# Kernel tuning notes

Hardware: AMD Instinct MI355X
Metric: run time of the kernel (lower is better)

The kernel has to match this reference:

```python
import jax, jax.numpy as jnp
import numpy as np


def bilinear_resize(x, out_h, out_w):
    # x: [B, C, H, W]; matches torch F.interpolate(mode='bilinear', align_corners=False)
    B, C, H, W = x.shape
    ry = jnp.clip((jnp.arange(out_h, dtype=jnp.float32) + 0.5) * (H / out_h) - 0.5, 0.0, H - 1)
    rx = jnp.clip((jnp.arange(out_w, dtype=jnp.float32) + 0.5) * (W / out_w) - 0.5, 0.0, W - 1)
    y0 = jnp.floor(ry).astype(jnp.int32); y1 = jnp.minimum(y0 + 1, H - 1)
    x0 = jnp.floor(rx).astype(jnp.int32); x1 = jnp.minimum(x0 + 1, W - 1)
    wy = (ry - y0)[:, None]  # [out_h,1]
    wx = (rx - x0)[None, :]  # [1,out_w]
    r0 = x[:, :, y0, :]; r1 = x[:, :, y1, :]
    v00 = r0[:, :, :, x0]; v01 = r0[:, :, :, x1]
    v10 = r1[:, :, :, x0]; v11 = r1[:, :, :, x1]
    return (v00 * (1 - wx) + v01 * wx) * (1 - wy) + (v10 * (1 - wx) + v11 * wx) * wy


def setup_inputs() -> dict:
    key0 = jax.random.key(0)
    ks = jax.random.split(key0, 16)
    B, N, C, H = 2, 300, 256, 8
    hw_lvl = np.array([[64, 64], [32, 32], [16, 16]], dtype=np.int64)
    L = int((hw_lvl[:, 0] * hw_lvl[:, 1]).sum())  # 5376
    p = lambda k, sh: (0.02 * jax.random.normal(k, sh, dtype=jnp.float32))
    return {
        'query': jax.random.normal(ks[0], (B, N, C), dtype=jnp.float32),
        'key': jax.random.normal(ks[1], (B, L, C), dtype=jnp.float32),
        'value': jax.random.normal(ks[2], (B, L, C), dtype=jnp.float32),
        'key_padding_mask': jnp.zeros((B, L), dtype=bool),
        'hw_lvl': hw_lvl,
        'Wq': p(ks[3], (C, C)), 'Wk': p(ks[4], (C, C)), 'Wv': p(ks[5], (C, C)),
        'Wp': p(ks[6], (C, C)), 'bp': jnp.zeros((C,), jnp.float32),
        'W1': p(ks[7], (H, H)), 'b1': jnp.zeros((H,), jnp.float32),
        'W2': p(ks[8], (H, H)), 'b2': jnp.zeros((H,), jnp.float32),
        'W3': p(ks[9], (H, H)), 'b3': jnp.zeros((H,), jnp.float32),
        'Wm': p(ks[10], (3 * H, 1)), 'bm': jnp.zeros((1,), jnp.float32),
    }


def reference(query, key, value, key_padding_mask, hw_lvl,
              Wq, Wk, Wv, Wp, bp, W1, b1, W2, b2, W3, b3, Wm, bm):
    hw = np.asarray(hw_lvl)
    h1, wd1 = int(hw[0, 0]), int(hw[0, 1])
    h2, wd2 = int(hw[1, 0]), int(hw[1, 1])
    h3, wd3 = int(hw[2, 0]), int(hw[2, 1])
    w1 = h1 * wd1
    w2 = w1 + h2 * wd2
    B, N, C = query.shape
    L = key.shape[1]
    H = W1.shape[0]
    scale = (C // H) ** -0.5

    q = (query @ Wq).reshape(B, N, H, C // H)
    k = (key @ Wk).reshape(B, L, H, C // H)
    v = (value @ Wv).reshape(B, L, H, C // H)
    attn = jnp.einsum('bnhd,blhd->bhnl', q, k) * scale  # [B,H,N,L]

    ap = attn.transpose(0, 2, 3, 1)  # [B,N,L,H]
    f1 = jax.nn.relu(ap[:, :, :w1] @ W1 + b1)                      # [B,N,w1,H]
    f2 = jax.nn.relu(ap[:, :, w1:w2] @ W2 + b2)                    # [B,N,h2*wd2,H]
    f3 = jax.nn.relu(ap[:, :, w2:] @ W3 + b3)                      # [B,N,h3*wd3,H]
    f2 = f2.transpose(0, 1, 3, 2).reshape(B * N, H, h2, wd2)
    f3 = f3.transpose(0, 1, 3, 2).reshape(B * N, H, h3, wd3)
    f2 = bilinear_resize(f2, h1, wd1).transpose(0, 2, 3, 1).reshape(B, N, w1, H)
    f3 = bilinear_resize(f3, h1, wd1).transpose(0, 2, 3, 1).reshape(B, N, w1, H)
    new_feats = jnp.concatenate([f1, f2, f3], axis=-1)             # [B,N,w1,3H]
    mask = jax.nn.relu(new_feats @ Wm + bm)                        # [B,N,w1,1]

    aw = jax.nn.softmax(attn, axis=-1)                             # [B,H,N,L]
    x = jnp.einsum('bhnl,blhd->bnhd', aw, v).reshape(B, N, C)
    x = x @ Wp + bp
    return x, mask
```

## Files before the change

kernel.cpp:

```cpp
#include <hip/hip_runtime.h>
#include <hip/hip_bf16.h>

typedef __hip_bfloat16 bf16;
typedef __attribute__((ext_vector_type(8))) short short8v;
typedef __attribute__((ext_vector_type(8))) unsigned short ushort8v;
typedef __attribute__((ext_vector_type(4))) unsigned short ushort4v;
typedef __attribute__((ext_vector_type(4))) float float4v;

__device__ __forceinline__ float bfu2f(unsigned short u) {
    union { unsigned int i; float f; } v; v.i = ((unsigned int)u) << 16; return v.f;
}
__device__ __forceinline__ unsigned short f2bfu_rn(float x) {
    union { float f; unsigned int i; } u; u.f = x;
    unsigned int r = (u.i + 0x7FFFu + ((u.i >> 16) & 1u)) >> 16;
    return (unsigned short)r;
}

__global__ __launch_bounds__(256) void cast_wt(
    const float* __restrict__ Wq, const float* __restrict__ Wk,
    const float* __restrict__ Wv, const float* __restrict__ Wp,
    unsigned short* __restrict__ wt)
{
    __shared__ unsigned short tile[64][72];
    const float* W = (blockIdx.z == 0) ? Wq : (blockIdx.z == 1) ? Wk
                   : (blockIdx.z == 2) ? Wv : Wp;
    unsigned short* WT = wt + (size_t)blockIdx.z * 65536;
    const int t = threadIdx.x;
    const int k0 = blockIdx.x * 64, n0 = blockIdx.y * 64;
    {
        const int r = t >> 2, cseg = (t & 3) * 16;
        const float* src = W + (size_t)(k0 + r) * 256 + n0 + cseg;
        #pragma unroll
        for (int j = 0; j < 16; ++j) tile[r][cseg + j] = f2bfu_rn(src[j]);
    }
    __syncthreads();
    {
        const int ch = t & 63, lq = t >> 6;
        ushort8v o0, o1;
        #pragma unroll
        for (int i = 0; i < 8; ++i) o0[i] = tile[lq * 16 + i][ch];
        #pragma unroll
        for (int i = 0; i < 8; ++i) o1[i] = tile[lq * 16 + 8 + i][ch];
        unsigned short* dst = WT + (size_t)(n0 + ch) * 256 + k0 + lq * 16;
        *(ushort8v*)(dst)     = o0;
        *(ushort8v*)(dst + 8) = o1;
    }
}

__device__ __forceinline__ void proj_core(
    const float* __restrict__ aptr, const unsigned short* __restrict__ Wt,
    int nc0, int m16, int quad, float4v acc[8])
{
    #pragma unroll
    for (int i = 0; i < 8; ++i) acc[i] = (float4v){0.f, 0.f, 0.f, 0.f};
    #pragma unroll
    for (int ks = 0; ks < 8; ++ks) {
        float4 a0 = *(const float4*)(aptr + ks * 32);
        float4 a1 = *(const float4*)(aptr + ks * 32 + 4);
        short8v af;
        af[0] = (short)f2bfu_rn(a0.x); af[1] = (short)f2bfu_rn(a0.y);
        af[2] = (short)f2bfu_rn(a0.z); af[3] = (short)f2bfu_rn(a0.w);
        af[4] = (short)f2bfu_rn(a1.x); af[5] = (short)f2bfu_rn(a1.y);
        af[6] = (short)f2bfu_rn(a1.z); af[7] = (short)f2bfu_rn(a1.w);
        #pragma unroll
        for (int i = 0; i < 8; ++i) {
            short8v bfr = *(const short8v*)(Wt + (size_t)(nc0 + i * 16 + m16) * 256 + ks * 32 + quad * 8);
            acc[i] = __builtin_amdgcn_mfma_f32_16x16x32_bf16(af, bfr, acc[i], 0, 0, 0);
        }
    }
}

__global__ __launch_bounds__(256) void proj_all(
    const float* __restrict__ q, const float* __restrict__ k, const float* __restrict__ v,
    const unsigned short* __restrict__ wt,
    unsigned short* __restrict__ qb, unsigned short* __restrict__ kb,
    unsigned short* __restrict__ vt)
{
    const int t = threadIdx.x;
    const int wave = t >> 6, lane = t & 63;
    const int m16 = lane & 15, quad = lane >> 4;
    const int msub = (wave & 1) * 16;
    const int nc0 = (wave >> 1) * 128;
    const int bx = blockIdx.x;

    float4v acc[8];
    if (bx < 19) {
        const int m0 = bx * 32;
        const int arow = min(m0 + msub + m16, 599);
        proj_core(q + (size_t)arow * 256 + quad * 8, wt, nc0, m16, quad, acc);
        #pragma unroll
        for (int i = 0; i < 8; ++i)
            #pragma unroll
            for (int r = 0; r < 4; ++r) {
                int m = m0 + msub + quad * 4 + r;
                if (m < 600)
                    qb[(size_t)m * 256 + nc0 + i * 16 + m16] = f2bfu_rn(acc[i][r]);
            }
    } else if (bx < 355) {
        const int m0 = (bx - 19) * 32;
        proj_core(k + (size_t)(m0 + msub + m16) * 256 + quad * 8, wt + 65536, nc0, m16, quad, acc);
        const int bb = (m0 >= 5376) ? 1 : 0;
        const int lb0 = m0 - bb * 5376 + msub + quad * 4;
        const int hbase = (wave >> 1) * 4;
        #pragma unroll
        for (int i = 0; i < 8; ++i) {
            const int hh = hbase + (i >> 1);
            const int c16 = (i & 1) * 16;
            unsigned short* kdst = kb + ((size_t)(bb * 8 + hh) * 5376 + lb0) * 32 + c16 + m16;
            #pragma unroll
            for (int r = 0; r < 4; ++r)
                kdst[(size_t)r * 32] = f2bfu_rn(acc[i][r]);
        }
    } else {
        const int m0 = (bx - 355) * 32;
        proj_core(v + (size_t)(m0 + msub + m16) * 256 + quad * 8, wt + 131072, nc0, m16, quad, acc);
        const int bb = (m0 >= 5376) ? 1 : 0;
        const int lb0 = m0 - bb * 5376 + msub + quad * 4;
        const int g0 = lb0 >> 3, e0 = lb0 & 7;
        const int hbase = (wave >> 1) * 4;
        #pragma unroll
        for (int i = 0; i < 8; ++i) {
            const int hh = hbase + (i >> 1);
            const int cc = (i & 1) * 16 + m16;
            ushort4v p;
            #pragma unroll
            for (int r = 0; r < 4; ++r) p[r] = f2bfu_rn(acc[i][r]);
            *(ushort4v*)(vt + (((size_t)(bb * 8 + hh) * 672 + g0) * 32 + cc) * 8 + e0) = p;
        }
    }
}

__global__ __launch_bounds__(512) void attn_fused(
    const unsigned short* __restrict__ qb, const unsigned short* __restrict__ kb,
    const unsigned short* __restrict__ vt,
    const float* __restrict__ W1, const float* __restrict__ b1,
    const float* __restrict__ W2, const float* __restrict__ b2,
    const float* __restrict__ W3, const float* __restrict__ b3,
    const float* __restrict__ Wm,
    float* __restrict__ xbp, float* __restrict__ Sp,
    float* __restrict__ g2, float* __restrict__ g3, float* __restrict__ maskp)
{
    __shared__ unsigned short probs[8][16 * 136];
    __shared__ float wT[64];
    __shared__ float blv[8], wmv[8];

    const int t = threadIdx.x;
    const int wave = t >> 6, lane = t & 63;

    const int i0 = blockIdx.x;
    const int m = (i0 & 7) * 200 + (i0 >> 3);
    if (m >= 1596) return;
    const int grp = m / 19, nt = m - grp * 19;
    const int b = grp / 42, zz = grp - b * 42;
    const int n0 = nt * 16;
    const int l0 = zz * 128;
    const int lvl = (zz >= 32) + (zz >= 40);

    const float* Wl = (lvl == 0) ? W1 : (lvl == 1) ? W2 : W3;
    const float* bl = (lvl == 0) ? b1 : (lvl == 1) ? b2 : b3;
    if (t < 64) wT[t] = Wl[(t & 7) * 8 + (t >> 3)];
    if (t < 8)  { blv[t] = bl[t]; wmv[t] = Wm[lvl * 8 + t]; }

    const int m16 = lane & 15, quad = lane >> 4;
    const int h = wave;
    const float scale = 0.17677669529663687f;

    const unsigned short* kbase = kb + ((size_t)(b * 8 + h) * 5376 + l0) * 32 + quad * 8;
    const unsigned short* vtb = vt + ((size_t)(b * 8 + h) * 672 + (l0 >> 3)) * 256 + quad * 256 + m16 * 8;
    unsigned short* const pw = &probs[wave][0];

    short8v vb[8];
    #pragma unroll
    for (int s = 0; s < 4; ++s) {
        vb[2 * s]     = *(const short8v*)(vtb + s * 1024);
        vb[2 * s + 1] = *(const short8v*)(vtb + s * 1024 + 128);
    }
    const short8v qfrag = *(const short8v*)(qb + (size_t)(b * 300 + min(n0 + m16, 299)) * 256 + h * 32 + quad * 8);

    #pragma unroll
    for (int i = 0; i < 8; ++i) {
        short8v kf = *(const short8v*)(kbase + (size_t)(i * 16 + m16) * 32);
        float4v c = {0.f, 0.f, 0.f, 0.f};
        c = __builtin_amdgcn_mfma_f32_16x16x32_bf16(kf, qfrag, c, 0, 0, 0);
        ushort4v pk;
        #pragma unroll
        for (int r = 0; r < 4; ++r) pk[r] = f2bfu_rn(c[r] * scale);
        *(ushort4v*)(pw + m16 * 136 + i * 16 + quad * 4) = pk;
    }

    float4v c0 = {0.f, 0.f, 0.f, 0.f};
    float4v c1 = {0.f, 0.f, 0.f, 0.f};
    float sm0 = 0.f, sm1 = 0.f;
    #pragma unroll
    for (int step = 0; step < 4; ++step) {
        const int lloc = step * 32 + quad * 8;
        ushort8v ua = *(const ushort8v*)(pw + m16 * 136 + lloc);
        short8v af;
        #pragma unroll
        for (int j = 0; j < 8; ++j) {
            float e = __expf(bfu2f(ua[j]));
            if (j & 1) sm1 += e; else sm0 += e;
            af[j] = (short)f2bfu_rn(e);
        }
        c0 = __builtin_amdgcn_mfma_f32_16x16x32_bf16(af, vb[2 * step],     c0, 0, 0, 0);
        c1 = __builtin_amdgcn_mfma_f32_16x16x32_bf16(af, vb[2 * step + 1], c1, 0, 0, 0);
    }

    float sm = sm0 + sm1;
    sm += __shfl_xor(sm, 16);
    sm += __shfl_xor(sm, 32);
    float* xplane = xbp + (size_t)zz * 153600;
    float* splane = Sp + (size_t)zz * 4800;
    if (lane < 16 && n0 + lane < 300)
        splane[(size_t)(b * 300 + n0 + lane) * 8 + h] = sm;
    #pragma unroll
    for (int r = 0; r < 4; ++r) {
        const int n = n0 + quad * 4 + r;
        if (n < 300) {
            float* o = xplane + (size_t)(b * 300 + n) * 256 + h * 32 + m16;
            o[0]  = c0[r];
            o[16] = c1[r];
        }
    }

    __syncthreads();

    {
        const int nl = t >> 5;
        const int n = n0 + nl;
        if (n < 300) {
            const int lb = (t & 31) * 4;
            ushort4v u[8];
            #pragma unroll
            for (int hp = 0; hp < 8; ++hp)
                u[hp] = *(const ushort4v*)(&probs[hp][nl * 136 + lb]);
            float4 o;
            float* op = (float*)&o;
            #pragma unroll
            for (int half = 0; half < 2; ++half) {
                float sv[2][8];
                #pragma unroll
                for (int pp = 0; pp < 2; ++pp)
                    #pragma unroll
                    for (int hp = 0; hp < 8; ++hp) sv[pp][hp] = bfu2f(u[hp][half * 2 + pp]);
                float f0 = 0.f, f1 = 0.f;
                #pragma unroll
                for (int hh = 0; hh < 8; ++hh) {
                    const float4 wA = *(const float4*)(&wT[hh * 8]);
                    const float4 wB = *(const float4*)(&wT[hh * 8 + 4]);
                    const float bb_ = blv[hh], wm_ = wmv[hh];
                    float a0 = bb_
                        + sv[0][0] * wA.x + sv[0][1] * wA.y + sv[0][2] * wA.z + sv[0][3] * wA.w
                        + sv[0][4] * wB.x + sv[0][5] * wB.y + sv[0][6] * wB.z + sv[0][7] * wB.w;
                    float a1 = bb_
                        + sv[1][0] * wA.x + sv[1][1] * wA.y + sv[1][2] * wA.z + sv[1][3] * wA.w
                        + sv[1][4] * wB.x + sv[1][5] * wB.y + sv[1][6] * wB.z + sv[1][7] * wB.w;
                    f0 += fmaxf(a0, 0.f) * wm_;
                    f1 += fmaxf(a1, 0.f) * wm_;
                }
                op[half * 2]     = f0;
                op[half * 2 + 1] = f1;
            }
            const size_t bn = (size_t)(b * 300 + n);
            const int p = l0 + lb;
            float* dst = (lvl == 0) ? maskp + bn * 4096 + p
                       : (lvl == 1) ? g2 + bn * 1024 + (p - 4096)
                       :              g3 + bn * 256  + (p - 5120);
            *(float4*)dst = o;
        }
    }
}

__global__ __launch_bounds__(256) void finish(
    const float* __restrict__ g2, const float* __restrict__ g3,
    const float* __restrict__ xbp, const float* __restrict__ Sp,
    float* __restrict__ xr, float* __restrict__ Sr,
    const float* __restrict__ bmp, float* __restrict__ out)
{
    const int t = threadIdx.x;
    if (blockIdx.x < 600) {
        __shared__ float gs[1280];
        __shared__ float bms;
        const int bn = blockIdx.x;
        if (t == 0) bms = bmp[0];
        ((float4v*)gs)[t] = ((const float4v*)(g2 + (size_t)bn * 1024))[t];
        if (t < 64) ((float4v*)(gs + 1024))[t] = ((const float4v*)(g3 + (size_t)bn * 256))[t];
        __syncthreads();

        float* mp = out + 153600 + (size_t)bn * 4096;
        #pragma unroll
        for (int it = 0; it < 4; ++it) {
            const int p0 = it * 1024 + t * 4;
            float4v mv = *(const float4v*)(mp + p0);
            float4v res;
            #pragma unroll
            for (int pp = 0; pp < 4; ++pp) {
                const int p = p0 + pp;
                const int Y = p >> 6, X = p & 63;
                float acc = mv[pp] + bms;
                {
                    float ry = fminf(fmaxf(0.5f * Y - 0.25f, 0.f), 31.f);
                    float rx = fminf(fmaxf(0.5f * X - 0.25f, 0.f), 31.f);
                    int y0 = (int)ry, x0 = (int)rx;
                    int y1 = min(y0 + 1, 31), x1 = min(x0 + 1, 31);
                    float wy = ry - (float)y0, wx = rx - (float)x0;
                    acc += (gs[y0 * 32 + x0] * (1.f - wx) + gs[y0 * 32 + x1] * wx) * (1.f - wy)
                         + (gs[y1 * 32 + x0] * (1.f - wx) + gs[y1 * 32 + x1] * wx) * wy;
                }
                {
                    float ry = fminf(fmaxf(0.25f * Y - 0.375f, 0.f), 15.f);
                    float rx = fminf(fmaxf(0.25f * X - 0.375f, 0.f), 15.f);
                    int y0 = (int)ry, x0 = (int)rx;
                    int y1 = min(y0 + 1, 15), x1 = min(x0 + 1, 15);
                    float wy = ry - (float)y0, wx = rx - (float)x0;
                    acc += (gs[1024 + y0 * 16 + x0] * (1.f - wx) + gs[1024 + y0 * 16 + x1] * wx) * (1.f - wy)
                         + (gs[1024 + y1 * 16 + x0] * (1.f - wx) + gs[1024 + y1 * 16 + x1] * wx) * wy;
                }
                res[pp] = fmaxf(acc, 0.f);
            }
            *(float4v*)(mp + p0) = res;
        }
    } else {
        const int idx = (blockIdx.x - 600) * 256 + t;
        if (idx < 38400) {
            float4v s = {0.f, 0.f, 0.f, 0.f};
            #pragma unroll 7
            for (int z = 0; z < 42; ++z)
                s += *(const float4v*)(xbp + (size_t)z * 153600 + (size_t)idx * 4);
            *(float4v*)(xr + (size_t)idx * 4) = s;
        } else if (idx < 38400 + 1200) {
            const int si = (idx - 38400) * 4;
            float4v s = {0.f, 0.f, 0.f, 0.f};
            #pragma unroll 7
            for (int z = 0; z < 42; ++z)
                s += *(const float4v*)(Sp + (size_t)z * 4800 + si);
            *(float4v*)(Sr + si) = s;
        }
    }
}

__global__ __launch_bounds__(256) void proj_out(
    const float* __restrict__ xr, const float* __restrict__ Sr,
    const unsigned short* __restrict__ Wtp,
    const float* __restrict__ bpv, float* __restrict__ out)
{
    const int t = threadIdx.x;
    const int wave = t >> 6, lane = t & 63;
    const int m16 = lane & 15, quad = lane >> 4;
    const int nc0 = wave * 64;
    const int m0 = blockIdx.x * 16;
    const int arow = min(m0 + m16, 599);
    const float* a0p = xr + (size_t)arow * 256 + quad * 8;

    float4v acc[4];
    #pragma unroll
    for (int i = 0; i < 4; ++i) acc[i] = (float4v){0.f, 0.f, 0.f, 0.f};

    #pragma unroll
    for (int ks = 0; ks < 8; ++ks) {
        const float rS = 1.0f / Sr[(size_t)arow * 8 + ks];
        float4 x0 = *(const float4*)(a0p + ks * 32);
        float4 x1 = *(const float4*)(a0p + ks * 32 + 4);
        short8v af;
        af[0] = (short)f2bfu_rn(x0.x * rS); af[1] = (short)f2bfu_rn(x0.y * rS);
        af[2] = (short)f2bfu_rn(x0.z * rS); af[3] = (short)f2bfu_rn(x0.w * rS);
        af[4] = (short)f2bfu_rn(x1.x * rS); af[5] = (short)f2bfu_rn(x1.y * rS);
        af[6] = (short)f2bfu_rn(x1.z * rS); af[7] = (short)f2bfu_rn(x1.w * rS);
        #pragma unroll
        for (int i = 0; i < 4; ++i) {
            short8v bfr = *(const short8v*)(Wtp + (size_t)(nc0 + i * 16 + m16) * 256 + ks * 32 + quad * 8);
            acc[i] = __builtin_amdgcn_mfma_f32_16x16x32_bf16(af, bfr, acc[i], 0, 0, 0);
        }
    }

    #pragma unroll
    for (int i = 0; i < 4; ++i) {
        const float bv = bpv[nc0 + i * 16 + m16];
        #pragma unroll
        for (int r = 0; r < 4; ++r) {
            int mm = m0 + quad * 4 + r;
            if (mm < 600)
                out[(size_t)mm * 256 + nc0 + i * 16 + m16] = acc[i][r] + bv;
        }
    }
}

extern "C" void kernel_launch(void* const* d_in, const int* in_sizes, int n_in,
                              void* d_out, int out_size, void* d_ws, size_t ws_size,
                              hipStream_t stream) {
    const float* query = (const float*)d_in[0];
    const float* key   = (const float*)d_in[1];
    const float* value = (const float*)d_in[2];
    const float* Wq = (const float*)d_in[5];
    const float* Wk = (const float*)d_in[6];
    const float* Wv = (const float*)d_in[7];
    const float* Wp = (const float*)d_in[8];
    const float* bp = (const float*)d_in[9];
    const float* W1 = (const float*)d_in[10];
    const float* b1 = (const float*)d_in[11];
    const float* W2 = (const float*)d_in[12];
    const float* b2 = (const float*)d_in[13];
    const float* W3 = (const float*)d_in[14];
    const float* b3 = (const float*)d_in[15];
    const float* Wm = (const float*)d_in[16];
    const float* bm = (const float*)d_in[17];
    float* out = (float*)d_out;

    char* ws = (char*)d_ws;
    unsigned short* wt = (unsigned short*)(ws);
    bf16*  qb   = (bf16*) (ws + 524288);
    bf16*  kb   = (bf16*) (ws + 831488);
    bf16*  vt   = (bf16*) (ws + 6336512);
    float* xbp  = (float*)(ws + 11841536);
    float* Sp   = (float*)(ws + 37646336);
    float* g2   = (float*)(ws + 38452736);
    float* g3   = (float*)(ws + 40910336);
    float* xr   = (float*)(ws + 41524736);
    float* Sr   = (float*)(ws + 42139136);
    float* maskp = out + 153600;

    cast_wt<<<dim3(4, 4, 4), 256, 0, stream>>>(Wq, Wk, Wv, Wp, wt);

    proj_all<<<691, 256, 0, stream>>>(query, key, value, wt,
        (unsigned short*)qb, (unsigned short*)kb, (unsigned short*)vt);

    attn_fused<<<1600, 512, 0, stream>>>(
        (const unsigned short*)qb, (const unsigned short*)kb, (const unsigned short*)vt,
        W1, b1, W2, b2, W3, b3, Wm, xbp, Sp, g2, g3, maskp);

    finish<<<755, 256, 0, stream>>>(g2, g3, xbp, Sp, xr, Sr, bm, out);

    proj_out<<<38, 256, 0, stream>>>(xr, Sr, (const unsigned short*)wt + 196608, bp, out);
}
```

Measured before the change: 179.6 us.

## Process two 128-key chunks per attention block to halve partial-sum planes

```diff
diff --git a/kernel.cpp b/kernel.cpp
--- a/kernel.cpp
+++ b/kernel.cpp
@@ -148,13 +148,13 @@
     const int wave = t >> 6, lane = t & 63;
 
     const int i0 = blockIdx.x;
-    const int m = (i0 & 7) * 200 + (i0 >> 3);
-    if (m >= 1596) return;
+    const int m = (i0 & 7) * 100 + (i0 >> 3);
+    if (m >= 798) return;
     const int grp = m / 19, nt = m - grp * 19;
-    const int b = grp / 42, zz = grp - b * 42;
+    const int b = grp / 21, zp = grp - b * 21;
     const int n0 = nt * 16;
-    const int l0 = zz * 128;
-    const int lvl = (zz >= 32) + (zz >= 40);
+    const int l0 = zp * 256;
+    const int lvl = (2 * zp >= 32) + (2 * zp >= 40);
 
     const float* Wl = (lvl == 0) ? W1 : (lvl == 1) ? W2 : W3;
     const float* bl = (lvl == 0) ? b1 : (lvl == 1) ? b2 : b3;
@@ -169,6 +169,50 @@
     const unsigned short* vtb = vt + ((size_t)(b * 8 + h) * 672 + (l0 >> 3)) * 256 + quad * 256 + m16 * 8;
     unsigned short* const pw = &probs[wave][0];
 
+    const int nl = t >> 5, lb = (t & 31) * 4;
+    const bool fold_act = (n0 + nl < 300);
+    const size_t bnf = (size_t)(b * 300 + n0 + nl);
+
+    auto do_fold = [&](int c) {
+        if (!fold_act) return;
+        ushort4v u[8];
+        #pragma unroll
+        for (int hp = 0; hp < 8; ++hp)
+            u[hp] = *(const ushort4v*)(&probs[hp][nl * 136 + lb]);
+        float4 o;
+        float* op = (float*)&o;
+        #pragma unroll
+        for (int half = 0; half < 2; ++half) {
+            float sv[2][8];
+            #pragma unroll
+            for (int pp = 0; pp < 2; ++pp)
+                #pragma unroll
+                for (int hp = 0; hp < 8; ++hp) sv[pp][hp] = bfu2f(u[hp][half * 2 + pp]);
+            float f0 = 0.f, f1 = 0.f;
+            #pragma unroll
+            for (int hh = 0; hh < 8; ++hh) {
+                const float4 wA = *(const float4*)(&wT[hh * 8]);
+                const float4 wB = *(const float4*)(&wT[hh * 8 + 4]);
+                const float bb_ = blv[hh], wm_ = wmv[hh];
+                float a0 = bb_
+                    + sv[0][0] * wA.x + sv[0][1] * wA.y + sv[0][2] * wA.z + sv[0][3] * wA.w
+                    + sv[0][4] * wB.x + sv[0][5] * wB.y + sv[0][6] * wB.z + sv[0][7] * wB.w;
+                float a1 = bb_
+                    + sv[1][0] * wA.x + sv[1][1] * wA.y + sv[1][2] * wA.z + sv[1][3] * wA.w
+                    + sv[1][4] * wB.x + sv[1][5] * wB.y + sv[1][6] * wB.z + sv[1][7] * wB.w;
+                f0 += fmaxf(a0, 0.f) * wm_;
+                f1 += fmaxf(a1, 0.f) * wm_;
+            }
+            op[half * 2]     = f0;
+            op[half * 2 + 1] = f1;
+        }
+        const int p = l0 + c * 128 + lb;
+        float* dst = (lvl == 0) ? maskp + bnf * 4096 + p
+                   : (lvl == 1) ? g2 + bnf * 1024 + (p - 4096)
+                   :              g3 + bnf * 256  + (p - 5120);
+        *(float4*)dst = o;
+    };
+
     short8v vb[8];
     #pragma unroll
     for (int s = 0; s < 4; ++s) {
@@ -176,6 +220,10 @@
         vb[2 * s + 1] = *(const short8v*)(vtb + s * 1024 + 128);
     }
     const short8v qfrag = *(const short8v*)(qb + (size_t)(b * 300 + min(n0 + m16, 299)) * 256 + h * 32 + quad * 8);
+
+    float4v c0 = {0.f, 0.f, 0.f, 0.f};
+    float4v c1 = {0.f, 0.f, 0.f, 0.f};
+    float sm0 = 0.f, sm1 = 0.f;
 
     #pragma unroll
     for (int i = 0; i < 8; ++i) {
@@ -187,10 +235,6 @@
         for (int r = 0; r < 4; ++r) pk[r] = f2bfu_rn(c[r] * scale);
         *(ushort4v*)(pw + m16 * 136 + i * 16 + quad * 4) = pk;
     }
-
-    float4v c0 = {0.f, 0.f, 0.f, 0.f};
-    float4v c1 = {0.f, 0.f, 0.f, 0.f};
-    float sm0 = 0.f, sm1 = 0.f;
     #pragma unroll
     for (int step = 0; step < 4; ++step) {
         const int lloc = step * 32 + quad * 8;
@@ -205,12 +249,49 @@
         c0 = __builtin_amdgcn_mfma_f32_16x16x32_bf16(af, vb[2 * step],     c0, 0, 0, 0);
         c1 = __builtin_amdgcn_mfma_f32_16x16x32_bf16(af, vb[2 * step + 1], c1, 0, 0, 0);
     }
+    #pragma unroll
+    for (int s = 0; s < 4; ++s) {
+        vb[2 * s]     = *(const short8v*)(vtb + 4096 + s * 1024);
+        vb[2 * s + 1] = *(const short8v*)(vtb + 4096 + s * 1024 + 128);
+    }
+
+    __syncthreads();
+    do_fold(0);
+    __syncthreads();
+
+    #pragma unroll
+    for (int i = 0; i < 8; ++i) {
+        short8v kf = *(const short8v*)(kbase + 4096 + (size_t)(i * 16 + m16) * 32);
+        float4v c = {0.f, 0.f, 0.f, 0.f};
+        c = __builtin_amdgcn_mfma_f32_16x16x32_bf16(kf, qfrag, c, 0, 0, 0);
+        ushort4v pk;
+        #pragma unroll
+        for (int r = 0; r < 4; ++r) pk[r] = f2bfu_rn(c[r] * scale);
+        *(ushort4v*)(pw + m16 * 136 + i * 16 + quad * 4) = pk;
+    }
+    #pragma unroll
+    for (int step = 0; step < 4; ++step) {
+        const int lloc = step * 32 + quad * 8;
+        ushort8v ua = *(const ushort8v*)(pw + m16 * 136 + lloc);
+        short8v af;
+        #pragma unroll
+        for (int j = 0; j < 8; ++j) {
+            float e = __expf(bfu2f(ua[j]));
+            if (j & 1) sm1 += e; else sm0 += e;
+            af[j] = (short)f2bfu_rn(e);
+        }
+        c0 = __builtin_amdgcn_mfma_f32_16x16x32_bf16(af, vb[2 * step],     c0, 0, 0, 0);
+        c1 = __builtin_amdgcn_mfma_f32_16x16x32_bf16(af, vb[2 * step + 1], c1, 0, 0, 0);
+    }
+
+    __syncthreads();
+    do_fold(1);
 
     float sm = sm0 + sm1;
     sm += __shfl_xor(sm, 16);
     sm += __shfl_xor(sm, 32);
-    float* xplane = xbp + (size_t)zz * 153600;
-    float* splane = Sp + (size_t)zz * 4800;
+    float* xplane = xbp + (size_t)zp * 153600;
+    float* splane = Sp + (size_t)zp * 4800;
     if (lane < 16 && n0 + lane < 300)
         splane[(size_t)(b * 300 + n0 + lane) * 8 + h] = sm;
     #pragma unroll
@@ -220,53 +301,6 @@
             float* o = xplane + (size_t)(b * 300 + n) * 256 + h * 32 + m16;
             o[0]  = c0[r];
             o[16] = c1[r];
-        }
-    }
-
-    __syncthreads();
-
-    {
-        const int nl = t >> 5;
-        const int n = n0 + nl;
-        if (n < 300) {
-            const int lb = (t & 31) * 4;
-            ushort4v u[8];
-            #pragma unroll
-            for (int hp = 0; hp < 8; ++hp)
-                u[hp] = *(const ushort4v*)(&probs[hp][nl * 136 + lb]);
-            float4 o;
-            float* op = (float*)&o;
-            #pragma unroll
-            for (int half = 0; half < 2; ++half) {
-                float sv[2][8];
-                #pragma unroll
-                for (int pp = 0; pp < 2; ++pp)
-                    #pragma unroll
-                    for (int hp = 0; hp < 8; ++hp) sv[pp][hp] = bfu2f(u[hp][half * 2 + pp]);
-                float f0 = 0.f, f1 = 0.f;
-                #pragma unroll
-                for (int hh = 0; hh < 8; ++hh) {
-                    const float4 wA = *(const float4*)(&wT[hh * 8]);
-                    const float4 wB = *(const float4*)(&wT[hh * 8 + 4]);
-                    const float bb_ = blv[hh], wm_ = wmv[hh];
-                    float a0 = bb_
-                        + sv[0][0] * wA.x + sv[0][1] * wA.y + sv[0][2] * wA.z + sv[0][3] * wA.w
-                        + sv[0][4] * wB.x + sv[0][5] * wB.y + sv[0][6] * wB.z + sv[0][7] * wB.w;
-                    float a1 = bb_
-                        + sv[1][0] * wA.x + sv[1][1] * wA.y + sv[1][2] * wA.z + sv[1][3] * wA.w
-                        + sv[1][4] * wB.x + sv[1][5] * wB.y + sv[1][6] * wB.z + sv[1][7] * wB.w;
-                    f0 += fmaxf(a0, 0.f) * wm_;
-                    f1 += fmaxf(a1, 0.f) * wm_;
-                }
-                op[half * 2]     = f0;
-                op[half * 2 + 1] = f1;
-            }
-            const size_t bn = (size_t)(b * 300 + n);
-            const int p = l0 + lb;
-            float* dst = (lvl == 0) ? maskp + bn * 4096 + p
-                       : (lvl == 1) ? g2 + bn * 1024 + (p - 4096)
-                       :              g3 + bn * 256  + (p - 5120);
-            *(float4*)dst = o;
         }
     }
 }
@@ -325,14 +359,14 @@
         if (idx < 38400) {
             float4v s = {0.f, 0.f, 0.f, 0.f};
             #pragma unroll 7
-            for (int z = 0; z < 42; ++z)
+            for (int z = 0; z < 21; ++z)
                 s += *(const float4v*)(xbp + (size_t)z * 153600 + (size_t)idx * 4);
             *(float4v*)(xr + (size_t)idx * 4) = s;
         } else if (idx < 38400 + 1200) {
             const int si = (idx - 38400) * 4;
             float4v s = {0.f, 0.f, 0.f, 0.f};
             #pragma unroll 7
-            for (int z = 0; z < 42; ++z)
+            for (int z = 0; z < 21; ++z)
                 s += *(const float4v*)(Sp + (size_t)z * 4800 + si);
             *(float4v*)(Sr + si) = s;
         }
@@ -412,11 +446,11 @@
     bf16*  kb   = (bf16*) (ws + 831488);
     bf16*  vt   = (bf16*) (ws + 6336512);
     float* xbp  = (float*)(ws + 11841536);
-    float* Sp   = (float*)(ws + 37646336);
-    float* g2   = (float*)(ws + 38452736);
-    float* g3   = (float*)(ws + 40910336);
-    float* xr   = (float*)(ws + 41524736);
-    float* Sr   = (float*)(ws + 42139136);
+    float* Sp   = (float*)(ws + 24743936);
+    float* g2   = (float*)(ws + 25147136);
+    float* g3   = (float*)(ws + 27604736);
+    float* xr   = (float*)(ws + 28219136);
+    float* Sr   = (float*)(ws + 28833536);
     float* maskp = out + 153600;
 
     cast_wt<<<dim3(4, 4, 4), 256, 0, stream>>>(Wq, Wk, Wv, Wp, wt);
@@ -424,7 +458,7 @@
     proj_all<<<691, 256, 0, stream>>>(query, key, value, wt,
         (unsigned short*)qb, (unsigned short*)kb, (unsigned short*)vt);
 
-    attn_fused<<<1600, 512, 0, stream>>>(
+    attn_fused<<<800, 512, 0, stream>>>(
         (const unsigned short*)qb, (const unsigned short*)kb, (const unsigned short*)vt,
         W1, b1, W2, b2, W3, b3, Wm, xbp, Sp, g2, g3, maskp);
 
```

Result: slower. 188.4 us (+4.9%).
